# Kernel tuning notes

Hardware: AMD Instinct MI355X
Metric: run time of the kernel (lower is better)

The kernel has to match this reference:

```python
import jax, jax.numpy as jnp
import numpy as np

B, N, D, DH = 2, 512, 64, 64


def _lin_params(key, din, dout):
    kw, kb = jax.random.split(key)
    bound = 1.0 / np.sqrt(din)
    W = jax.random.uniform(kw, (din, dout), jnp.float32, -bound, bound)
    b = jax.random.uniform(kb, (dout,), jnp.float32, -bound, bound)
    return W, b


def setup_inputs() -> dict:
    key = jax.random.key(0)
    ks = jax.random.split(key, 11)
    inp = {
        "x": jax.random.normal(ks[0], (B, N, D), jnp.float32),
        "e": jax.random.normal(ks[1], (B, N, N, D), jnp.float32),
    }
    # node-to-node self-attention: Linear(d, d_head)
    inp["Wq1"], inp["bq1"] = _lin_params(ks[2], D, DH)
    inp["Wk1"], inp["bk1"] = _lin_params(ks[3], D, DH)
    inp["Wv1"], inp["bv1"] = _lin_params(ks[4], D, DH)
    # node-to-edge cross-attention
    inp["Wqe"], inp["bqe"] = _lin_params(ks[5], D, DH)   # Q_edge: Linear(d, d_head) on e
    inp["Wkn"], inp["bkn"] = _lin_params(ks[6], DH, DH)  # K_node: Linear(d_head, d_head)
    inp["Wvn"], inp["bvn"] = _lin_params(ks[7], DH, DH)  # V_node
    # edge-to-node cross-attention (all Linear(d_head, d_head))
    inp["Wqn"], inp["bqn"] = _lin_params(ks[8], DH, DH)
    inp["Wke"], inp["bke"] = _lin_params(ks[9], DH, DH)
    inp["Wve"], inp["bve"] = _lin_params(ks[10], DH, DH)
    return inp


def _forward(x, e, Wq1, bq1, Wk1, bk1, Wv1, bv1,
             Wqe, bqe, Wkn, bkn, Wvn, bvn,
             Wqn, bqn, Wke, bke, Wve, bve):
    sqrt_d = jnp.sqrt(jnp.asarray(DH, x.dtype))
    lin = lambda z, W, b: z @ W + b

    # --- self-attention node-to-node: x (B,N,d) -> x_hat (B,N,d_head) ---
    Q = lin(x, Wq1, bq1)
    K = lin(x, Wk1, bk1)
    V = lin(x, Wv1, bv1)
    A = jax.nn.softmax(jnp.einsum('bnd,bmd->bnm', Q, K) / sqrt_d, axis=-1)
    x_hat = jnp.einsum('bnm,bmd->bnd', A, V)

    # --- cross-attention node-to-edge: update e (B,N,N,d) -> e_new (B,N,N,d_head) ---
    Qe = lin(e, Wqe, bqe)                 # (B,N,N,dh)
    Kn = lin(x_hat, Wkn, bkn)             # (B,N,dh)
    Vn = lin(x_hat, Wvn, bvn)
    Si = jnp.einsum('bijd,bjd->bij', Qe, Kn) / sqrt_d  # K_i[b,i,j] = Kn[b,j]
    Sj = jnp.einsum('bijd,bid->bij', Qe, Kn) / sqrt_d  # K_j[b,i,j] = Kn[b,i]
    # Att_i/(Att_i+Att_j) = sigmoid(Si - Sj)
    Ai = jax.nn.sigmoid(Si - Sj)
    Aj = 1.0 - Ai
    e_new = Ai[..., None] * Vn[:, None, :, :] + Aj[..., None] * Vn[:, :, None, :]

    # --- cross-attention edge-to-node: x_new (B,N,d_head) ---
    Qn = lin(x_hat, Wqn, bqn)             # (B,N,dh)
    Ke = lin(e_new, Wke, bke)             # (B,N,N,dh)
    Ve = lin(e_new, Wve, bve)
    S = jnp.einsum('bid,bijd->bij', Qn, Ke) / sqrt_d
    A2 = jax.nn.softmax(S, axis=2)
    x_new = jnp.einsum('bij,bijd->bid', A2, Ve)
    return x_new, e_new


def reference(x, e, Wq1, bq1, Wk1, bk1, Wv1, bv1,
              Wqe, bqe, Wkn, bkn, Wvn, bvn,
              Wqn, bqn, Wke, bke, Wve, bve):
    return _forward(x, e, Wq1, bq1, Wk1, bk1, Wv1, bv1,
                    Wqe, bqe, Wkn, bkn, Wvn, bvn,
                    Wqn, bqn, Wke, bke, Wve, bve)
```

## Files before the change

kernel.cpp:

```cpp
#include <hip/hip_runtime.h>
#include <math.h>

#define NN 512
#define RR 1024

typedef float f4 __attribute__((ext_vector_type(4)));

__global__ __launch_bounds__(256) void prep_kernel(
    const float* __restrict__ x,
    const float* __restrict__ Wq1, const float* __restrict__ bq1,
    const float* __restrict__ Wk1, const float* __restrict__ bk1,
    const float* __restrict__ Wv1, const float* __restrict__ bv1,
    const float* __restrict__ Wkn, const float* __restrict__ bkn,
    const float* __restrict__ Wvn, const float* __restrict__ bvn,
    const float* __restrict__ Wqe, const float* __restrict__ bqe,
    const float* __restrict__ Wke, const float* __restrict__ Wve,
    float* __restrict__ Q, float* __restrict__ K, float* __restrict__ V,
    float* __restrict__ M_P, float* __restrict__ c_P,
    float* __restrict__ M_ke, float* __restrict__ c_ke,
    float* __restrict__ M_ve, float* __restrict__ c_ve,
    float* __restrict__ vq0, float* __restrict__ s0p)
{
    __shared__ float sh[14528];
    const int t = threadIdx.x;

    if (blockIdx.x < 3) {
        const int m = blockIdx.x;
        float* As = sh;
        float* Bs = sh + 4160;
        float* va = sh + 8320;
        float* vb = sh + 8384;
        const float* A  = (m == 0) ? Wkn : Wvn;
        const float* aV = (m == 0) ? bkn : bvn;
        const float* B  = (m == 0) ? Wqe : (m == 1 ? Wke : Wve);
#pragma unroll
        for (int p = 0; p < 16; ++p) {
            const int idx = p * 256 + t;
            const int r = idx >> 6, cc = idx & 63;
            As[r * 65 + cc] = A[idx];
            if (m == 0) Bs[r * 65 + cc] = B[idx];
            else        Bs[cc * 65 + r] = B[idx];
        }
        if (t < 64) { va[t] = aV[t]; vb[t] = bqe[t]; }
        __syncthreads();

        const int b = t & 63, g = t >> 6;
        float acc[16];
#pragma unroll
        for (int aa = 0; aa < 16; ++aa) acc[aa] = 0.f;
        for (int k = 0; k < 64; ++k) {
            const float bv = Bs[b * 65 + k];
#pragma unroll
            for (int aa = 0; aa < 16; ++aa)
                acc[aa] = fmaf(As[(g * 16 + aa) * 65 + k], bv, acc[aa]);
        }
        float* M = (m == 0) ? M_P : (m == 1 ? M_ke : M_ve);
#pragma unroll
        for (int aa = 0; aa < 16; ++aa)
            M[(g * 16 + aa) * 64 + b] = acc[aa];

        if (t < 64) {
            float cb = 0.f;
            for (int k = 0; k < 64; ++k) cb = fmaf(va[k], Bs[t * 65 + k], cb);
            float* C = (m == 0) ? c_P : (m == 1 ? c_ke : c_ve);
            C[t] = cb;
            if (m == 0) {
                float q = 0.f;
                for (int k = 0; k < 64; ++k) q = fmaf(As[t * 65 + k], vb[k], q);
                vq0[t] = q * 0.125f;
            }
        }
        if (m == 0 && t == 0) {
            float s = 0.f;
            for (int k = 0; k < 64; ++k) s += vb[k] * va[k];
            *s0p = s * 0.125f;
        }
    } else {
        const int rb = (blockIdx.x - 3) * 32;
        float* Ws0 = sh;
        float* Ws1 = sh + 4096;
        float* Ws2 = sh + 8192;
        float* xs  = sh + 12288;
        float* bs0 = sh + 14336;
        float* bs1 = sh + 14400;
        float* bs2 = sh + 14464;
#pragma unroll
        for (int p = 0; p < 4; ++p) {
            const int idx = p * 256 + t;
            ((f4*)Ws0)[idx] = ((const f4*)Wq1)[idx];
            ((f4*)Ws1)[idx] = ((const f4*)Wk1)[idx];
            ((f4*)Ws2)[idx] = ((const f4*)Wv1)[idx];
        }
        ((f4*)xs)[t]       = ((const f4*)(x + rb * 64))[t];
        ((f4*)xs)[t + 256] = ((const f4*)(x + rb * 64))[t + 256];
        if (t < 64) { bs0[t] = bq1[t]; bs1[t] = bk1[t]; bs2[t] = bv1[t]; }
        __syncthreads();

        const int d = t & 63, g = t >> 6;
        float a0[8], a1[8], a2[8];
#pragma unroll
        for (int r = 0; r < 8; ++r) { a0[r] = bs0[d]; a1[r] = bs1[d]; a2[r] = bs2[d]; }
        for (int k4 = 0; k4 < 16; ++k4) {
            float w0[4], w1[4], w2[4];
#pragma unroll
            for (int kk = 0; kk < 4; ++kk) {
                w0[kk] = Ws0[(k4 * 4 + kk) * 64 + d];
                w1[kk] = Ws1[(k4 * 4 + kk) * 64 + d];
                w2[kk] = Ws2[(k4 * 4 + kk) * 64 + d];
            }
#pragma unroll
            for (int r = 0; r < 8; ++r) {
                const f4 xv = ((const f4*)xs)[(g * 8 + r) * 16 + k4];
                a0[r] = fmaf(xv.x, w0[0], fmaf(xv.y, w0[1], fmaf(xv.z, w0[2], fmaf(xv.w, w0[3], a0[r]))));
                a1[r] = fmaf(xv.x, w1[0], fmaf(xv.y, w1[1], fmaf(xv.z, w1[2], fmaf(xv.w, w1[3], a1[r]))));
                a2[r] = fmaf(xv.x, w2[0], fmaf(xv.y, w2[1], fmaf(xv.z, w2[2], fmaf(xv.w, w2[3], a2[r]))));
            }
        }
#pragma unroll
        for (int r = 0; r < 8; ++r) {
            Q[(rb + g * 8 + r) * 64 + d] = a0[r];
            K[(rb + g * 8 + r) * 64 + d] = a1[r];
            V[(rb + g * 8 + r) * 64 + d] = a2[r];
        }
    }
}

__global__ __launch_bounds__(512) void selfattn_kernel(
    const float* __restrict__ Q, const float* __restrict__ K,
    const float* __restrict__ V, float* __restrict__ xhat)
{
    const int row = blockIdx.x;
    const int b = row >> 9;
    const int t = threadIdx.x;
    __shared__ float qr[64];
    __shared__ float p[512];
    __shared__ float red[512];
    if (t < 64) qr[t] = Q[row * 64 + t];
    __syncthreads();

    {
        const int m = t;
        const f4* kr = (const f4*)(K + (size_t)(b * NN + m) * 64);
        const f4* qq = (const f4*)qr;
        float sp[4] = {0.f, 0.f, 0.f, 0.f};
#pragma unroll
        for (int u = 0; u < 16; ++u) {
            const f4 w = kr[u];
            const f4 qv = qq[u];
            sp[u & 3] += qv.x * w.x + qv.y * w.y + qv.z * w.z + qv.w * w.w;
        }
        p[m] = ((sp[0] + sp[1]) + (sp[2] + sp[3])) * 0.125f;
    }
    __syncthreads();

    const int lane = t & 63, w = t >> 6;
    const float v0 = p[t];
    float m = v0;
#pragma unroll
    for (int o = 1; o < 64; o <<= 1) m = fmaxf(m, __shfl_xor(m, o));
    if (lane == 0) red[w] = m;
    __syncthreads();
    float mx = red[0];
#pragma unroll
    for (int z = 1; z < 8; ++z) mx = fmaxf(mx, red[z]);
    const float e0 = expf(v0 - mx);
    float ss = e0;
#pragma unroll
    for (int o = 1; o < 64; o <<= 1) ss += __shfl_xor(ss, o);
    if (lane == 0) red[8 + w] = ss;
    __syncthreads();
    const float inv = 1.f / (red[8] + red[9] + red[10] + red[11]
                           + red[12] + red[13] + red[14] + red[15]);
    p[t] = e0;
    __syncthreads();

    const int d = t & 63, q = t >> 6;
    float acc = 0.f;
    const int j0 = q * 64;
    for (int j = j0; j < j0 + 64; ++j)
        acc = fmaf(p[j], V[(b * NN + j) * 64 + d], acc);
    red[t] = acc;
    __syncthreads();
    if (t < 64) {
        float s8 = 0.f;
#pragma unroll
        for (int z = 0; z < 8; ++z) s8 += red[t + z * 64];
        xhat[row * 64 + t] = s8 * inv;
    }
}

__global__ __launch_bounds__(256) void affine5_kernel(
    const float* __restrict__ xhat,
    const float* __restrict__ Wqn, const float* __restrict__ bqn,
    const float* __restrict__ Wvn, const float* __restrict__ bvn,
    const float* __restrict__ M_P, const float* __restrict__ c_P,
    const float* __restrict__ M_ke, const float* __restrict__ c_ke,
    const float* __restrict__ M_ve, const float* __restrict__ c_ve,
    const float* __restrict__ vq0, const float* __restrict__ s0p,
    float* __restrict__ Qn, float* __restrict__ Vn, float* __restrict__ P,
    float* __restrict__ VnWke, float* __restrict__ VnWve, float* __restrict__ q0)
{
    const int t = threadIdx.x;
    const int rb = blockIdx.x * 32;
    const int m = blockIdx.y;
    const float* W; const float* c; float* o;
    if (m == 0)      { W = Wqn;  c = bqn;  o = Qn; }
    else if (m == 1) { W = Wvn;  c = bvn;  o = Vn; }
    else if (m == 2) { W = M_P;  c = c_P;  o = P; }
    else if (m == 3) { W = M_ke; c = c_ke; o = VnWke; }
    else             { W = M_ve; c = c_ve; o = VnWve; }
    __shared__ float Ws[4096], xs[2048], cs[64], vq0s[64];
#pragma unroll
    for (int p = 0; p < 4; ++p) ((f4*)Ws)[p * 256 + t] = ((const f4*)W)[p * 256 + t];
    ((f4*)xs)[t]       = ((const f4*)(xhat + rb * 64))[t];
    ((f4*)xs)[t + 256] = ((const f4*)(xhat + rb * 64))[t + 256];
    if (t < 64) { cs[t] = c[t]; if (m == 0) vq0s[t] = vq0[t]; }
    __syncthreads();

    const int d = t & 63, g = t >> 6;
    float acc[8];
#pragma unroll
    for (int r = 0; r < 8; ++r) acc[r] = cs[d];
    for (int k4 = 0; k4 < 16; ++k4) {
        float w[4];
#pragma unroll
        for (int kk = 0; kk < 4; ++kk) w[kk] = Ws[(k4 * 4 + kk) * 64 + d];
#pragma unroll
        for (int r = 0; r < 8; ++r) {
            const f4 xv = ((const f4*)xs)[(g * 8 + r) * 16 + k4];
            acc[r] = fmaf(xv.x, w[0], fmaf(xv.y, w[1], fmaf(xv.z, w[2], fmaf(xv.w, w[3], acc[r]))));
        }
    }
#pragma unroll
    for (int r = 0; r < 8; ++r) o[(rb + g * 8 + r) * 64 + d] = acc[r];

    if (m == 0) {
        const int row = t >> 3, seg = t & 7;
        float part = 0.f;
#pragma unroll
        for (int kk = 0; kk < 8; ++kk)
            part = fmaf(xs[row * 64 + seg * 8 + kk], vq0s[seg * 8 + kk], part);
        part += __shfl_xor(part, 1);
        part += __shfl_xor(part, 2);
        part += __shfl_xor(part, 4);
        if (seg == 0) q0[rb + row] = part + s0p[0];
    }
}

__global__ __launch_bounds__(256) void edge_kernel(
    const float* __restrict__ e, const float* __restrict__ P,
    const float* __restrict__ q0, const float* __restrict__ Vn,
    const float* __restrict__ Qn, const float* __restrict__ VnWke,
    const float* __restrict__ VnWve,
    float* __restrict__ e_new,
    float* __restrict__ Epart, float* __restrict__ Gpart, float* __restrict__ Wpart)
{
    const int blk = blockIdx.x;
    const int bi = blk >> 3;
    const int jc = blk & 7;
    const int b  = bi >> 9;
    const int t  = threadIdx.x;
    const int r  = t >> 4;
    const int k  = t & 15;

    const float q0i = q0[bi];
    const f4 pi4 = ((const f4*)P)[bi * 16 + k];
    const f4 vi4 = ((const f4*)Vn)[bi * 16 + k];
    const f4 qn4 = ((const f4*)Qn)[bi * 16 + k];
    const f4 wi4 = ((const f4*)VnWke)[bi * 16 + k];
    float uii = qn4.x * wi4.x + qn4.y * wi4.y + qn4.z * wi4.z + qn4.w * wi4.w;
    uii += __shfl_xor(uii, 1);
    uii += __shfl_xor(uii, 2);
    uii += __shfl_xor(uii, 4);
    uii += __shfl_xor(uii, 8);
    uii *= 0.125f;

    const f4* erow  = (const f4*)(e     + (size_t)bi * NN * 64);
    f4*       enrow = (f4*)      (e_new + (size_t)bi * NN * 64);
    const f4* Prow  = (const f4*)P     + (size_t)b * NN * 16;
    const f4* Vrow  = (const f4*)Vn    + (size_t)b * NN * 16;
    const f4* Krow  = (const f4*)VnWke + (size_t)b * NN * 16;
    const f4* Wvrow = (const f4*)VnWve + (size_t)b * NN * 16;
    const float* q0b = q0 + b * NN;

    float Eacc = 0.f, Gacc = 0.f;
    f4 Wacc = {0.f, 0.f, 0.f, 0.f};

#pragma unroll
    for (int it = 0; it < 4; ++it) {
        const int j = jc * 64 + it * 16 + r;
        const f4 ev = erow[j * 16 + k];
        const f4 pj = Prow[j * 16 + k];
        const f4 wj = Krow[j * 16 + k];
        float s = ev.x * (pj.x - pi4.x) + ev.y * (pj.y - pi4.y)
                + ev.z * (pj.z - pi4.z) + ev.w * (pj.w - pi4.w);
        float uu = qn4.x * wj.x + qn4.y * wj.y + qn4.z * wj.z + qn4.w * wj.w;
        s  += __shfl_xor(s, 1);  uu += __shfl_xor(uu, 1);
        s  += __shfl_xor(s, 2);  uu += __shfl_xor(uu, 2);
        s  += __shfl_xor(s, 4);  uu += __shfl_xor(uu, 4);
        s  += __shfl_xor(s, 8);  uu += __shfl_xor(uu, 8);
        const float ai = 1.f / (1.f + expf(-(s * 0.125f + q0b[j] - q0i)));
        const f4 vj = Vrow[j * 16 + k];
        f4 en;
        en.x = fmaf(ai, vj.x - vi4.x, vi4.x);
        en.y = fmaf(ai, vj.y - vi4.y, vi4.y);
        en.z = fmaf(ai, vj.z - vi4.z, vi4.z);
        en.w = fmaf(ai, vj.w - vi4.w, vi4.w);
        __builtin_nontemporal_store(en, enrow + j * 16 + k);

        const float ex  = expf(ai * (uu * 0.125f - uii));
        const float aex = ai * ex;
        Eacc += ex;
        Gacc += aex;
        const f4 wv = Wvrow[j * 16 + k];
        Wacc.x = fmaf(aex, wv.x, Wacc.x);
        Wacc.y = fmaf(aex, wv.y, Wacc.y);
        Wacc.z = fmaf(aex, wv.z, Wacc.z);
        Wacc.w = fmaf(aex, wv.w, Wacc.w);
    }

    Eacc += __shfl_xor(Eacc, 16);  Eacc += __shfl_xor(Eacc, 32);
    Gacc += __shfl_xor(Gacc, 16);  Gacc += __shfl_xor(Gacc, 32);
    Wacc.x += __shfl_xor(Wacc.x, 16);  Wacc.x += __shfl_xor(Wacc.x, 32);
    Wacc.y += __shfl_xor(Wacc.y, 16);  Wacc.y += __shfl_xor(Wacc.y, 32);
    Wacc.z += __shfl_xor(Wacc.z, 16);  Wacc.z += __shfl_xor(Wacc.z, 32);
    Wacc.w += __shfl_xor(Wacc.w, 16);  Wacc.w += __shfl_xor(Wacc.w, 32);

    __shared__ float Wred[4][65];
    __shared__ float EG[8];
    const int l = t & 63, w = t >> 6;
    if (l < 16) {
        Wred[w][l * 4 + 0] = Wacc.x;
        Wred[w][l * 4 + 1] = Wacc.y;
        Wred[w][l * 4 + 2] = Wacc.z;
        Wred[w][l * 4 + 3] = Wacc.w;
        if (l == 0) { EG[w] = Eacc; EG[4 + w] = Gacc; }
    }
    __syncthreads();
    if (t < 64) {
        const float Wsum = Wred[0][t] + Wred[1][t] + Wred[2][t] + Wred[3][t];
        Wpart[((size_t)jc * RR + bi) * 64 + t] = Wsum;
        if (t == 0) {
            Epart[jc * RR + bi] = EG[0] + EG[1] + EG[2] + EG[3];
            Gpart[jc * RR + bi] = EG[4] + EG[5] + EG[6] + EG[7];
        }
    }
}

__global__ __launch_bounds__(64) void final_kernel(
    const float* __restrict__ Epart, const float* __restrict__ Gpart,
    const float* __restrict__ Wpart, const float* __restrict__ VnWve,
    const float* __restrict__ bve, float* __restrict__ x_new)
{
    const int bi = blockIdx.x;
    const int t = threadIdx.x;
    float Wsum = 0.f;
#pragma unroll
    for (int jc = 0; jc < 8; ++jc)
        Wsum += Wpart[((size_t)jc * RR + bi) * 64 + t];
    float E = 0.f, G = 0.f;
#pragma unroll
    for (int jc = 0; jc < 8; ++jc) {
        E += Epart[jc * RR + bi];
        G += Gpart[jc * RR + bi];
    }
    const float inv = 1.f / E;
    x_new[(size_t)bi * 64 + t] = bve[t] + VnWve[(size_t)bi * 64 + t] * (1.f - G * inv)
                               + Wsum * inv;
}

extern "C" void kernel_launch(void* const* d_in, const int* in_sizes, int n_in,
                              void* d_out, int out_size, void* d_ws, size_t ws_size,
                              hipStream_t stream) {
    const float* x   = (const float*)d_in[0];
    const float* e   = (const float*)d_in[1];
    const float* Wq1 = (const float*)d_in[2];  const float* bq1 = (const float*)d_in[3];
    const float* Wk1 = (const float*)d_in[4];  const float* bk1 = (const float*)d_in[5];
    const float* Wv1 = (const float*)d_in[6];  const float* bv1 = (const float*)d_in[7];
    const float* Wqe = (const float*)d_in[8];  const float* bqe = (const float*)d_in[9];
    const float* Wkn = (const float*)d_in[10]; const float* bkn = (const float*)d_in[11];
    const float* Wvn = (const float*)d_in[12]; const float* bvn = (const float*)d_in[13];
    const float* Wqn = (const float*)d_in[14]; const float* bqn = (const float*)d_in[15];
    const float* Wke = (const float*)d_in[16];
    const float* Wve = (const float*)d_in[18]; const float* bve = (const float*)d_in[19];

    float* out = (float*)d_out;
    float* x_new = out;
    float* e_new = out + 2 * NN * 64;

    float* ws = (float*)d_ws;
    float* Q     = ws;
    float* K     = Q + RR * 64;
    float* V     = K + RR * 64;
    float* xhat  = V + RR * 64;
    float* Qn    = xhat + RR * 64;
    float* Vn    = Qn + RR * 64;
    float* P     = Vn + RR * 64;
    float* VnWke = P + RR * 64;
    float* VnWve = VnWke + RR * 64;
    float* q0    = VnWve + RR * 64;
    float* M_P   = q0 + RR;
    float* M_ke  = M_P + 4096;
    float* M_ve  = M_ke + 4096;
    float* c_P   = M_ve + 4096;
    float* c_ke  = c_P + 64;
    float* c_ve  = c_ke + 64;
    float* vq0   = c_ve + 64;
    float* s0    = vq0 + 64;
    float* Epart = s0 + 64;
    float* Gpart = Epart + 8 * RR;
    float* Wpart = Gpart + 8 * RR;

    prep_kernel<<<35, 256, 0, stream>>>(x, Wq1, bq1, Wk1, bk1, Wv1, bv1,
                                        Wkn, bkn, Wvn, bvn, Wqe, bqe, Wke, Wve,
                                        Q, K, V,
                                        M_P, c_P, M_ke, c_ke, M_ve, c_ve, vq0, s0);
    selfattn_kernel<<<RR, 512, 0, stream>>>(Q, K, V, xhat);
    affine5_kernel<<<dim3(32, 5), 256, 0, stream>>>(xhat, Wqn, bqn, Wvn, bvn,
                                                    M_P, c_P, M_ke, c_ke, M_ve, c_ve,
                                                    vq0, s0,
                                                    Qn, Vn, P, VnWke, VnWve, q0);
    edge_kernel<<<RR * 8, 256, 0, stream>>>(e, P, q0, Vn, Qn, VnWke, VnWve,
                                            e_new, Epart, Gpart, Wpart);
    final_kernel<<<RR, 64, 0, stream>>>(Epart, Gpart, Wpart, VnWve, bve, x_new);
}
```

Before: 95.11 us.

## Split fused edge kernel into ai, e_new and x_new kernels via stored sigmoid weights

```diff
diff --git a/kernel.cpp b/kernel.cpp
--- a/kernel.cpp
+++ b/kernel.cpp
@@ -247,13 +247,9 @@
     }
 }
 
-__global__ __launch_bounds__(256) void edge_kernel(
+__global__ __launch_bounds__(256) void ai_kernel(
     const float* __restrict__ e, const float* __restrict__ P,
-    const float* __restrict__ q0, const float* __restrict__ Vn,
-    const float* __restrict__ Qn, const float* __restrict__ VnWke,
-    const float* __restrict__ VnWve,
-    float* __restrict__ e_new,
-    float* __restrict__ Epart, float* __restrict__ Gpart, float* __restrict__ Wpart)
+    const float* __restrict__ q0, float* __restrict__ AiB)
 {
     const int blk = blockIdx.x;
     const int bi = blk >> 3;
@@ -265,41 +261,48 @@
 
     const float q0i = q0[bi];
     const f4 pi4 = ((const f4*)P)[bi * 16 + k];
-    const f4 vi4 = ((const f4*)Vn)[bi * 16 + k];
-    const f4 qn4 = ((const f4*)Qn)[bi * 16 + k];
-    const f4 wi4 = ((const f4*)VnWke)[bi * 16 + k];
-    float uii = qn4.x * wi4.x + qn4.y * wi4.y + qn4.z * wi4.z + qn4.w * wi4.w;
-    uii += __shfl_xor(uii, 1);
-    uii += __shfl_xor(uii, 2);
-    uii += __shfl_xor(uii, 4);
-    uii += __shfl_xor(uii, 8);
-    uii *= 0.125f;
-
-    const f4* erow  = (const f4*)(e     + (size_t)bi * NN * 64);
-    f4*       enrow = (f4*)      (e_new + (size_t)bi * NN * 64);
-    const f4* Prow  = (const f4*)P     + (size_t)b * NN * 16;
-    const f4* Vrow  = (const f4*)Vn    + (size_t)b * NN * 16;
-    const f4* Krow  = (const f4*)VnWke + (size_t)b * NN * 16;
-    const f4* Wvrow = (const f4*)VnWve + (size_t)b * NN * 16;
+    const f4* erow = (const f4*)(e + (size_t)bi * NN * 64);
+    const f4* Prow = (const f4*)P + (size_t)b * NN * 16;
     const float* q0b = q0 + b * NN;
-
-    float Eacc = 0.f, Gacc = 0.f;
-    f4 Wacc = {0.f, 0.f, 0.f, 0.f};
+    float* aiout = AiB + (size_t)bi * NN;
 
 #pragma unroll
     for (int it = 0; it < 4; ++it) {
         const int j = jc * 64 + it * 16 + r;
         const f4 ev = erow[j * 16 + k];
         const f4 pj = Prow[j * 16 + k];
-        const f4 wj = Krow[j * 16 + k];
         float s = ev.x * (pj.x - pi4.x) + ev.y * (pj.y - pi4.y)
                 + ev.z * (pj.z - pi4.z) + ev.w * (pj.w - pi4.w);
-        float uu = qn4.x * wj.x + qn4.y * wj.y + qn4.z * wj.z + qn4.w * wj.w;
-        s  += __shfl_xor(s, 1);  uu += __shfl_xor(uu, 1);
-        s  += __shfl_xor(s, 2);  uu += __shfl_xor(uu, 2);
-        s  += __shfl_xor(s, 4);  uu += __shfl_xor(uu, 4);
-        s  += __shfl_xor(s, 8);  uu += __shfl_xor(uu, 8);
-        const float ai = 1.f / (1.f + expf(-(s * 0.125f + q0b[j] - q0i)));
+        s += __shfl_xor(s, 1);
+        s += __shfl_xor(s, 2);
+        s += __shfl_xor(s, 4);
+        s += __shfl_xor(s, 8);
+        if (k == 0)
+            aiout[j] = 1.f / (1.f + expf(-(s * 0.125f + q0b[j] - q0i)));
+    }
+}
+
+__global__ __launch_bounds__(256) void enew_kernel(
+    const float* __restrict__ AiB, const float* __restrict__ Vn,
+    float* __restrict__ e_new)
+{
+    const int blk = blockIdx.x;
+    const int bi = blk >> 3;
+    const int jc = blk & 7;
+    const int b  = bi >> 9;
+    const int t  = threadIdx.x;
+    const int r  = t >> 4;
+    const int k  = t & 15;
+
+    const f4 vi4 = ((const f4*)Vn)[bi * 16 + k];
+    const f4* Vrow = (const f4*)Vn + (size_t)b * NN * 16;
+    const float* aiin = AiB + (size_t)bi * NN;
+    f4* enrow = (f4*)(e_new + (size_t)bi * NN * 64);
+
+#pragma unroll
+    for (int it = 0; it < 4; ++it) {
+        const int j = jc * 64 + it * 16 + r;
+        const float ai = aiin[j];
         const f4 vj = Vrow[j * 16 + k];
         f4 en;
         en.x = fmaf(ai, vj.x - vi4.x, vi4.x);
@@ -307,66 +310,77 @@
         en.z = fmaf(ai, vj.z - vi4.z, vi4.z);
         en.w = fmaf(ai, vj.w - vi4.w, vi4.w);
         __builtin_nontemporal_store(en, enrow + j * 16 + k);
-
-        const float ex  = expf(ai * (uu * 0.125f - uii));
-        const float aex = ai * ex;
-        Eacc += ex;
-        Gacc += aex;
-        const f4 wv = Wvrow[j * 16 + k];
-        Wacc.x = fmaf(aex, wv.x, Wacc.x);
-        Wacc.y = fmaf(aex, wv.y, Wacc.y);
-        Wacc.z = fmaf(aex, wv.z, Wacc.z);
-        Wacc.w = fmaf(aex, wv.w, Wacc.w);
-    }
-
-    Eacc += __shfl_xor(Eacc, 16);  Eacc += __shfl_xor(Eacc, 32);
-    Gacc += __shfl_xor(Gacc, 16);  Gacc += __shfl_xor(Gacc, 32);
-    Wacc.x += __shfl_xor(Wacc.x, 16);  Wacc.x += __shfl_xor(Wacc.x, 32);
-    Wacc.y += __shfl_xor(Wacc.y, 16);  Wacc.y += __shfl_xor(Wacc.y, 32);
-    Wacc.z += __shfl_xor(Wacc.z, 16);  Wacc.z += __shfl_xor(Wacc.z, 32);
-    Wacc.w += __shfl_xor(Wacc.w, 16);  Wacc.w += __shfl_xor(Wacc.w, 32);
-
-    __shared__ float Wred[4][65];
-    __shared__ float EG[8];
-    const int l = t & 63, w = t >> 6;
-    if (l < 16) {
-        Wred[w][l * 4 + 0] = Wacc.x;
-        Wred[w][l * 4 + 1] = Wacc.y;
-        Wred[w][l * 4 + 2] = Wacc.z;
-        Wred[w][l * 4 + 3] = Wacc.w;
-        if (l == 0) { EG[w] = Eacc; EG[4 + w] = Gacc; }
-    }
+    }
+}
+
+__global__ __launch_bounds__(256) void xnew_kernel(
+    const float* __restrict__ AiB, const float* __restrict__ Qn,
+    const float* __restrict__ VnWke, const float* __restrict__ VnWve,
+    const float* __restrict__ bve, float* __restrict__ x_new)
+{
+    const int bi = blockIdx.x;
+    const int b = bi >> 9, i = bi & 511;
+    const int t = threadIdx.x;
+
+    __shared__ float qn[64];
+    __shared__ float us[512], as_[512], cs[512];
+    __shared__ float red[256];
+
+    if (t < 64) qn[t] = Qn[bi * 64 + t];
+    as_[t]       = AiB[(size_t)bi * NN + t];
+    as_[t + 256] = AiB[(size_t)bi * NN + t + 256];
+    __syncthreads();
+
+    {
+        const int j4 = t >> 2, l = t & 3;
+        const float4* qq = (const float4*)qn;
+#pragma unroll
+        for (int pass = 0; pass < 4; ++pass) {
+            const int j = pass * 128 + j4;
+            const float4* wr = (const float4*)(VnWke + (size_t)(b * NN + j) * 64) + l * 4;
+            float s = 0.f;
+#pragma unroll
+            for (int kk = 0; kk < 4; ++kk) {
+                const float4 w = wr[kk];
+                const float4 qv = qq[l * 4 + kk];
+                s += qv.x * w.x + qv.y * w.y + qv.z * w.z + qv.w * w.w;
+            }
+            s += __shfl_xor(s, 1);
+            s += __shfl_xor(s, 2);
+            if (l == 0) us[j] = s * 0.125f;
+        }
+    }
+    __syncthreads();
+
+    const int lane = t & 63, w = t >> 6;
+    const float uii = us[i];
+    const float a0 = as_[t], a1 = as_[t + 256];
+    const float ex0 = expf(a0 * (us[t] - uii));
+    const float ex1 = expf(a1 * (us[t + 256] - uii));
+    const float aex0 = a0 * ex0, aex1 = a1 * ex1;
+    cs[t] = aex0; cs[t + 256] = aex1;
+    float se = ex0 + ex1, sg = aex0 + aex1;
+#pragma unroll
+    for (int o = 1; o < 64; o <<= 1) { se += __shfl_xor(se, o); sg += __shfl_xor(sg, o); }
+    if (lane == 0) { red[w] = se; red[4 + w] = sg; }
+    __syncthreads();
+    const float E = red[0] + red[1] + red[2] + red[3];
+    const float G = red[4] + red[5] + red[6] + red[7];
+    const float inv = 1.f / E;
+    __syncthreads();
+
+    const int d = t & 63, q = t >> 6;
+    float acc = 0.f;
+    const int j0 = q * 128;
+    for (int j = j0; j < j0 + 128; ++j)
+        acc = fmaf(cs[j], VnWve[(b * NN + j) * 64 + d], acc);
+    red[t] = acc;
     __syncthreads();
     if (t < 64) {
-        const float Wsum = Wred[0][t] + Wred[1][t] + Wred[2][t] + Wred[3][t];
-        Wpart[((size_t)jc * RR + bi) * 64 + t] = Wsum;
-        if (t == 0) {
-            Epart[jc * RR + bi] = EG[0] + EG[1] + EG[2] + EG[3];
-            Gpart[jc * RR + bi] = EG[4] + EG[5] + EG[6] + EG[7];
-        }
-    }
-}
-
-__global__ __launch_bounds__(64) void final_kernel(
-    const float* __restrict__ Epart, const float* __restrict__ Gpart,
-    const float* __restrict__ Wpart, const float* __restrict__ VnWve,
-    const float* __restrict__ bve, float* __restrict__ x_new)
-{
-    const int bi = blockIdx.x;
-    const int t = threadIdx.x;
-    float Wsum = 0.f;
-#pragma unroll
-    for (int jc = 0; jc < 8; ++jc)
-        Wsum += Wpart[((size_t)jc * RR + bi) * 64 + t];
-    float E = 0.f, G = 0.f;
-#pragma unroll
-    for (int jc = 0; jc < 8; ++jc) {
-        E += Epart[jc * RR + bi];
-        G += Gpart[jc * RR + bi];
-    }
-    const float inv = 1.f / E;
-    x_new[(size_t)bi * 64 + t] = bve[t] + VnWve[(size_t)bi * 64 + t] * (1.f - G * inv)
-                               + Wsum * inv;
+        const float s4 = red[t] + red[t + 64] + red[t + 128] + red[t + 192];
+        x_new[(size_t)bi * 64 + t] = bve[t] + VnWve[(size_t)bi * 64 + t] * (1.f - G * inv)
+                                   + s4 * inv;
+    }
 }
 
 extern "C" void kernel_launch(void* const* d_in, const int* in_sizes, int n_in,
@@ -407,9 +421,7 @@
     float* c_ve  = c_ke + 64;
     float* vq0   = c_ve + 64;
     float* s0    = vq0 + 64;
-    float* Epart = s0 + 64;
-    float* Gpart = Epart + 8 * RR;
-    float* Wpart = Gpart + 8 * RR;
+    float* AiB   = s0 + 64;
 
     prep_kernel<<<35, 256, 0, stream>>>(x, Wq1, bq1, Wk1, bk1, Wv1, bv1,
                                         Wkn, bkn, Wvn, bvn, Wqe, bqe, Wke, Wve,
@@ -420,7 +432,7 @@
                                                     M_P, c_P, M_ke, c_ke, M_ve, c_ve,
                                                     vq0, s0,
                                                     Qn, Vn, P, VnWke, VnWve, q0);
-    edge_kernel<<<RR * 8, 256, 0, stream>>>(e, P, q0, Vn, Qn, VnWke, VnWve,
-                                            e_new, Epart, Gpart, Wpart);
-    final_kernel<<<RR, 64, 0, stream>>>(Epart, Gpart, Wpart, VnWve, bve, x_new);
-}
+    ai_kernel<<<RR * 8, 256, 0, stream>>>(e, P, q0, AiB);
+    enew_kernel<<<RR * 8, 256, 0, stream>>>(AiB, Vn, e_new);
+    xnew_kernel<<<RR, 256, 0, stream>>>(AiB, Qn, VnWke, VnWve, bve, x_new);
+}
```

After: 106.7 us. +12.1%, slower.
